# Kernel tuning notes

Hardware: AMD Instinct MI355X
Metric: run time of the kernel (lower is better)

## Reference

```python
import jax, jax.numpy as jnp
import numpy as np

D_MODEL = 1024
N_HEAD = 16
D_K = 64
D_V = 64
LN_EPS = 1e-5


def setup_inputs() -> dict:
    key = jax.random.key(0)
    ks = jax.random.split(key, 12)
    B, S = 4, 2048
    s = 1.0 / np.sqrt(D_MODEL)
    inp = {
        "q": jax.random.normal(ks[0], (B, S, D_MODEL), jnp.float32),
        "k": jax.random.normal(ks[1], (B, S, D_MODEL), jnp.float32),
        "v": jax.random.normal(ks[2], (B, S, D_MODEL), jnp.float32),
        "mask": jnp.ones((B, S, S), jnp.int32),
        "w_q": jax.random.normal(ks[3], (D_MODEL, N_HEAD * D_K), jnp.float32) * s,
        "b_q": jnp.zeros((N_HEAD * D_K,), jnp.float32),
        "w_k": jax.random.normal(ks[4], (D_MODEL, N_HEAD * D_K), jnp.float32) * s,
        "b_k": jnp.zeros((N_HEAD * D_K,), jnp.float32),
        "w_v": jax.random.normal(ks[5], (D_MODEL, N_HEAD * D_V), jnp.float32) * s,
        "b_v": jnp.zeros((N_HEAD * D_V,), jnp.float32),
        "w_fc": jax.random.normal(ks[6], (N_HEAD * D_V, D_MODEL), jnp.float32) * s,
        "b_fc": jnp.zeros((D_MODEL,), jnp.float32),
        "ln_g": jnp.ones((D_MODEL,), jnp.float32),
        "ln_b": jnp.zeros((D_MODEL,), jnp.float32),
    }
    return inp


def reference(q, k, v, mask, w_q, b_q, w_k, b_k, w_v, b_v, w_fc, b_fc, ln_g, ln_b):
    B, Sq, _ = q.shape
    Sk = k.shape[1]
    residual = q
    # QKV projections -> [B, H, S, d]
    qh = (q @ w_q + b_q).reshape(B, Sq, N_HEAD, D_K).transpose(0, 2, 1, 3)
    kh = (k @ w_k + b_k).reshape(B, Sk, N_HEAD, D_K).transpose(0, 2, 1, 3)
    vh = (v @ w_v + b_v).reshape(B, Sk, N_HEAD, D_V).transpose(0, 2, 1, 3)
    temp = jnp.sqrt(jnp.asarray(D_K, qh.dtype))
    scores = jnp.einsum("bhqd,bhkd->bhqk", qh / temp, kh)
    scores = jnp.where(mask[:, None, :, :] == 0, jnp.asarray(-1e9, scores.dtype), scores)
    attn = jax.nn.softmax(scores, axis=-1)  # dropout is identity in eval
    out = jnp.einsum("bhqk,bhkd->bhqd", attn, vh)
    out = out.transpose(0, 2, 1, 3).reshape(B, Sq, N_HEAD * D_V)
    out = out @ w_fc + b_fc  # output proj (dropout identity)
    x = out + residual
    mu = jnp.mean(x, axis=-1, keepdims=True)
    var = jnp.mean(jnp.square(x - mu), axis=-1, keepdims=True)
    y = (x - mu) * jax.lax.rsqrt(var + LN_EPS) * ln_g + ln_b
    return (y, attn)
```

## Files before the change

kernel.cpp:

```cpp
#include <hip/hip_runtime.h>
#include <cstdint>
#include <cstddef>

#define DM 1024
#define HN 16
#define DH 64
#define BB 4
#define SS 2048
#define MM (BB * SS)

typedef __bf16 bf16;
typedef bf16 bf16x8 __attribute__((ext_vector_type(8)));
typedef bf16 bf16x4 __attribute__((ext_vector_type(4)));
typedef float f32x4 __attribute__((ext_vector_type(4)));
typedef int i32x4 __attribute__((ext_vector_type(4)));

__device__ __forceinline__ f32x4 mfma16(bf16x8 a, bf16x8 b, f32x4 c) {
  return __builtin_amdgcn_mfma_f32_16x16x32_bf16(a, b, c, 0, 0, 0);
}

typedef __attribute__((address_space(3))) void lds_void_t;
typedef __attribute__((address_space(1))) void glob_void_t;

__device__ __forceinline__ void gload16(const void* g, void* l) {
  __builtin_amdgcn_global_load_lds((const glob_void_t*)g, (lds_void_t*)l, 16, 0, 0);
}

__global__ __launch_bounds__(256) void cvt3(const float* __restrict__ q,
                                            const float* __restrict__ k,
                                            const float* __restrict__ v,
                                            bf16* __restrict__ dst) {
  int which = blockIdx.y;
  const float* in = which == 0 ? q : which == 1 ? k : v;
  bf16* out = dst + (size_t)which * MM * DM;
  int i = (blockIdx.x * 256 + threadIdx.x) * 8;
  f32x4 a = *(const f32x4*)(in + i);
  f32x4 b = *(const f32x4*)(in + i + 4);
  bf16x8 o;
  o[0] = (bf16)a[0]; o[1] = (bf16)a[1]; o[2] = (bf16)a[2]; o[3] = (bf16)a[3];
  o[4] = (bf16)b[0]; o[5] = (bf16)b[1]; o[6] = (bf16)b[2]; o[7] = (bf16)b[3];
  *(bf16x8*)(out + i) = o;
}

__global__ __launch_bounds__(256) void wtrans4(const float* __restrict__ w_q,
                                               const float* __restrict__ w_k,
                                               const float* __restrict__ w_v,
                                               const float* __restrict__ w_fc,
                                               bf16* __restrict__ WT) {
  int p = blockIdx.z;
  const float* W = p == 0 ? w_q : p == 1 ? w_k : p == 2 ? w_v : w_fc;
  bf16* out = WT + (size_t)p * DM * DM;
  __shared__ float t[32][33];
  int n0 = blockIdx.x * 32, k0 = blockIdx.y * 32;
  int tid = threadIdx.x;
  int r = tid >> 3, c = (tid & 7) * 4;
  f32x4 v = *(const f32x4*)&W[(size_t)(k0 + r) * DM + n0 + c];
  t[r][c] = v[0]; t[r][c + 1] = v[1]; t[r][c + 2] = v[2]; t[r][c + 3] = v[3];
  __syncthreads();
  bf16x4 o;
#pragma unroll
  for (int i = 0; i < 4; ++i) o[i] = (bf16)t[c + i][r];
  *(bf16x4*)&out[(size_t)(n0 + r) * DM + k0 + c] = o;
}

__global__ __launch_bounds__(256) void gemm_qkv(const bf16* __restrict__ Abase,
                                                const bf16* __restrict__ Bt,
                                                const float* __restrict__ b_q,
                                                const float* __restrict__ b_k,
                                                const float* __restrict__ b_v,
                                                bf16* __restrict__ qhh,
                                                bf16* __restrict__ khh,
                                                bf16* __restrict__ vhT) {
  constexpr int K = DM;
  __shared__ bf16 Ab[128 * 32];
  __shared__ bf16 Bb[128 * 32];
  int tid = threadIdx.x, wave = tid >> 6, lane = tid & 63;
  int bm = blockIdx.x * 128, bn = blockIdx.y * 128;
  int proj = bn >> 10;
  const bf16* A = Abase + (size_t)proj * MM * DM;
  const float* bias = proj == 0 ? b_q : proj == 1 ? b_k : b_v;
  int wr = (wave >> 1) * 64, wc = (wave & 1) * 64;
  int fr = lane & 15, kg8 = (lane >> 4) * 8;
  f32x4 acc[4][4] = {};
  int arow = tid >> 2, acol = (tid & 3) * 8;
  const bf16* Ag0 = A + (size_t)(bm + arow) * K + acol;
  const bf16* Ag1 = Ag0 + (size_t)64 * K;
  const bf16* Bg0 = Bt + (size_t)(bn + arow) * K + acol;
  const bf16* Bg1 = Bg0 + (size_t)64 * K;
  char* la = (char*)Ab + wave * 1024;
  char* lb = (char*)Bb + wave * 1024;
  for (int k0 = 0; k0 < K; k0 += 32) {
    __syncthreads();
    gload16(Ag0 + k0, la);
    gload16(Ag1 + k0, la + 4096);
    gload16(Bg0 + k0, lb);
    gload16(Bg1 + k0, lb + 4096);
    asm volatile("s_waitcnt vmcnt(0)" ::: "memory");
    __syncthreads();
    bf16x8 af[4], bfr[4];
#pragma unroll
    for (int m = 0; m < 4; ++m)
      af[m] = *(const bf16x8*)&Ab[(wr + m * 16 + fr) * 32 + kg8];
#pragma unroll
    for (int n = 0; n < 4; ++n)
      bfr[n] = *(const bf16x8*)&Bb[(wc + n * 16 + fr) * 32 + kg8];
#pragma unroll
    for (int m = 0; m < 4; ++m)
#pragma unroll
      for (int n = 0; n < 4; ++n) acc[m][n] = mfma16(af[m], bfr[n], acc[m][n]);
  }
  int b = bm >> 11;
#pragma unroll
  for (int m = 0; m < 4; ++m)
#pragma unroll
    for (int n = 0; n < 4; ++n) {
      int c = bn + wc + n * 16 + fr;
      int lc = c & 1023;
      float bv = bias[lc];
      int h = lc >> 6, d = lc & 63;
      int r0 = bm + wr + m * 16 + (lane >> 4) * 4;
      int s0 = r0 & (SS - 1);
      if (proj == 2) {
        bf16x4 o;
#pragma unroll
        for (int j = 0; j < 4; ++j) o[j] = (bf16)(acc[m][n][j] + bv);
        *(bf16x4*)&vhT[((size_t)(b * HN + h) * DH + d) * SS + s0] = o;
      } else {
        bf16* dst = proj == 0 ? qhh : khh;
        float sc = proj == 0 ? 0.125f : 1.f;
#pragma unroll
        for (int j = 0; j < 4; ++j) {
          float v = (acc[m][n][j] + bv) * sc;
          dst[(size_t)(b * HN + h) * (SS * DH) + (size_t)(s0 + j) * DH + d] =
              (bf16)v;
        }
      }
    }
}

__global__ __launch_bounds__(256) void gemm_out(const bf16* __restrict__ A,
                                                const bf16* __restrict__ Bt,
                                                const float* __restrict__ bias,
                                                const float* __restrict__ resid,
                                                float* __restrict__ out) {
  constexpr int K = DM;
  __shared__ bf16 Ab[128 * 32];
  __shared__ bf16 Bb[128 * 32];
  int tid = threadIdx.x, wave = tid >> 6, lane = tid & 63;
  int bm = blockIdx.x * 128, bn = blockIdx.y * 128;
  int wr = (wave >> 1) * 64, wc = (wave & 1) * 64;
  int fr = lane & 15, kg8 = (lane >> 4) * 8;
  f32x4 acc[4][4] = {};
  int arow = tid >> 2, acol = (tid & 3) * 8;
  const bf16* Ag0 = A + (size_t)(bm + arow) * K + acol;
  const bf16* Ag1 = Ag0 + (size_t)64 * K;
  const bf16* Bg0 = Bt + (size_t)(bn + arow) * K + acol;
  const bf16* Bg1 = Bg0 + (size_t)64 * K;
  char* la = (char*)Ab + wave * 1024;
  char* lb = (char*)Bb + wave * 1024;
  for (int k0 = 0; k0 < K; k0 += 32) {
    __syncthreads();
    gload16(Ag0 + k0, la);
    gload16(Ag1 + k0, la + 4096);
    gload16(Bg0 + k0, lb);
    gload16(Bg1 + k0, lb + 4096);
    asm volatile("s_waitcnt vmcnt(0)" ::: "memory");
    __syncthreads();
    bf16x8 af[4], bfr[4];
#pragma unroll
    for (int m = 0; m < 4; ++m)
      af[m] = *(const bf16x8*)&Ab[(wr + m * 16 + fr) * 32 + kg8];
#pragma unroll
    for (int n = 0; n < 4; ++n)
      bfr[n] = *(const bf16x8*)&Bb[(wc + n * 16 + fr) * 32 + kg8];
#pragma unroll
    for (int m = 0; m < 4; ++m)
#pragma unroll
      for (int n = 0; n < 4; ++n) acc[m][n] = mfma16(af[m], bfr[n], acc[m][n]);
  }
#pragma unroll
  for (int m = 0; m < 4; ++m)
#pragma unroll
    for (int n = 0; n < 4; ++n) {
      int c = bn + wc + n * 16 + fr;
      float bv = bias[c];
#pragma unroll
      for (int j = 0; j < 4; ++j) {
        int r = bm + wr + m * 16 + (lane >> 4) * 4 + j;
        size_t idx = (size_t)r * DM + c;
        out[idx] = acc[m][n][j] + bv + resid[idx];
      }
    }
}

__global__ __launch_bounds__(512, 4) void attn_kernel(
    const bf16* __restrict__ qh, const bf16* __restrict__ kh,
    const bf16* __restrict__ vhT, const int* __restrict__ mask,
    float* __restrict__ attn_out, bf16* __restrict__ ctx) {
  extern __shared__ char smem[];
  float* pbuf = (float*)(smem + 16 * 4096);
  float* invp = (float*)(smem + 16 * 4096 + 4096);
  int tid = threadIdx.x, wave = tid >> 6, lane = tid & 63;
  int qt = blockIdx.x, bh = blockIdx.y;
  int b = bh >> 4, h = bh & 15;
  int q0 = qt * 16;
  const bf16* qbase = qh + ((size_t)bh * SS + q0) * DH;
  const bf16* kbase = kh + (size_t)bh * SS * DH;
  const bf16* vbase = vhT + (size_t)bh * SS * DH;
  int fr = lane & 15, kg = lane >> 4;

  bf16x8 qf0 = *(const bf16x8*)&qbase[(size_t)fr * DH + kg * 8];
  bf16x8 qf1 = *(const bf16x8*)&qbase[(size_t)fr * DH + 32 + kg * 8];

  {
    int sw = wave * 256;
    bf16x8 kb0[4], kb1[4];
    auto kload = [&](int g) {
      const bf16* kp = kbase + (size_t)(sw + g * 16 + fr) * DH + kg * 8;
      kb0[g & 3] = *(const bf16x8*)kp;
      kb1[g & 3] = *(const bf16x8*)(kp + 32);
    };
    kload(0);
    kload(1);
    kload(2);
#pragma unroll
    for (int g = 0; g < 16; ++g) {
      if (g < 13) kload(g + 3);
      f32x4 acc = {0.f, 0.f, 0.f, 0.f};
      acc = mfma16(qf0, kb0[g & 3], acc);
      acc = mfma16(qf1, kb1[g & 3], acc);
      int col = sw + g * 16 + fr;
      int slot = col >> 3, within = col & 7;
#pragma unroll
      for (int j = 0; j < 4; ++j) {
        int row = kg * 4 + j;
        *(bf16*)(smem + row * 4096 + ((slot ^ row) << 4) + within * 2) =
            (bf16)acc[j];
      }
    }
  }
  __syncthreads();

  {
    int row = wave * 2 + (lane >> 5);
    int la = lane & 31;
    char* rbase = smem + row * 4096;
    const int* mrow = mask + ((size_t)b * SS + q0 + row) * SS;
    float sum = 0.f;
#pragma unroll
    for (int it = 0; it < 8; ++it) {
      int slot = la + it * 32;
      char* p = rbase + ((slot ^ row) << 4);
      bf16x8 e = *(const bf16x8*)p;
      i32x4 ma = *(const i32x4*)&mrow[slot * 8];
      i32x4 mb = *(const i32x4*)&mrow[slot * 8 + 4];
      bf16x8 w8;
#pragma unroll
      for (int i = 0; i < 4; ++i) {
        float f = __expf((float)e[i]);
        f = (ma[i] == 0) ? 0.f : f;
        sum += f;
        w8[i] = (bf16)f;
      }
#pragma unroll
      for (int i = 0; i < 4; ++i) {
        float f = __expf((float)e[i + 4]);
        f = (mb[i] == 0) ? 0.f : f;
        sum += f;
        w8[i + 4] = (bf16)f;
      }
      *(bf16x8*)p = w8;
    }
#pragma unroll
    for (int off = 1; off < 32; off <<= 1) sum += __shfl_xor(sum, off);
    float inv = 1.f / sum;
    if (la == 0) invp[row] = inv;
    float* arow_ = attn_out + ((size_t)bh * SS + q0 + row) * SS;
#pragma unroll
    for (int it = 0; it < 8; ++it) {
      int slot = la + it * 32;
      bf16x8 e = *(const bf16x8*)(rbase + ((slot ^ row) << 4));
      f32x4 u0, u1;
#pragma unroll
      for (int i = 0; i < 4; ++i) {
        u0[i] = (float)e[i] * inv;
        u1[i] = (float)e[i + 4] * inv;
      }
      __builtin_nontemporal_store(u0, (f32x4*)&arow_[slot * 8]);
      __builtin_nontemporal_store(u1, (f32x4*)&arow_[slot * 8 + 4]);
    }
  }
  __syncthreads();

  {
    int dq = wave & 3, khalf = wave >> 2;
    f32x4 cacc = {0.f, 0.f, 0.f, 0.f};
    const bf16* vrow = vbase + (size_t)(dq * 16 + fr) * SS + khalf * 1024;
    char* prow = smem + fr * 4096;
    bf16x8 vb[4], pb[4];
    auto pvload = [&](int kk) {
      vb[kk & 3] = *(const bf16x8*)&vrow[kk * 32 + kg * 8];
      int slotA = khalf * 128 + kk * 4 + kg;
      pb[kk & 3] = *(const bf16x8*)(prow + ((slotA ^ fr) << 4));
    };
    pvload(0);
    pvload(1);
    pvload(2);
#pragma unroll
    for (int kk = 0; kk < 32; ++kk) {
      if (kk < 29) pvload(kk + 3);
      cacc = mfma16(pb[kk & 3], vb[kk & 3], cacc);
    }
    if (khalf == 1) {
#pragma unroll
      for (int j = 0; j < 4; ++j)
        pbuf[dq * 256 + (kg * 4 + j) * 16 + fr] = cacc[j];
    }
    __syncthreads();
    if (khalf == 0) {
#pragma unroll
      for (int j = 0; j < 4; ++j) {
        int row = kg * 4 + j;
        float v = (cacc[j] + pbuf[dq * 256 + row * 16 + fr]) * invp[row];
        ctx[((size_t)b * SS + q0 + row) * DM + h * DH + dq * 16 + fr] = (bf16)v;
      }
    }
  }
}

__global__ __launch_bounds__(256) void ln_k(float* __restrict__ x,
                                            const float* __restrict__ g,
                                            const float* __restrict__ bln) {
  int r = blockIdx.x, tid = threadIdx.x;
  f32x4 v = *(const f32x4*)&x[(size_t)r * DM + tid * 4];
  float s = v[0] + v[1] + v[2] + v[3];
  float s2 = v[0] * v[0] + v[1] * v[1] + v[2] * v[2] + v[3] * v[3];
#pragma unroll
  for (int off = 32; off; off >>= 1) {
    s += __shfl_down(s, off);
    s2 += __shfl_down(s2, off);
  }
  __shared__ float rs_[4], rs2_[4];
  int wave = tid >> 6, lane = tid & 63;
  if (lane == 0) {
    rs_[wave] = s;
    rs2_[wave] = s2;
  }
  __syncthreads();
  s = rs_[0] + rs_[1] + rs_[2] + rs_[3];
  s2 = rs2_[0] + rs2_[1] + rs2_[2] + rs2_[3];
  float mu = s * (1.f / DM);
  float var = s2 * (1.f / DM) - mu * mu;
  float rstd = rsqrtf(var + 1e-5f);
  f32x4 gg = *(const f32x4*)&g[tid * 4];
  f32x4 bb = *(const f32x4*)&bln[tid * 4];
  f32x4 o;
#pragma unroll
  for (int i = 0; i < 4; ++i) o[i] = (v[i] - mu) * rstd * gg[i] + bb[i];
  *(f32x4*)&x[(size_t)r * DM + tid * 4] = o;
}

extern "C" void kernel_launch(void* const* d_in, const int* in_sizes, int n_in,
                              void* d_out, int out_size, void* d_ws,
                              size_t ws_size, hipStream_t stream) {
  const float* q = (const float*)d_in[0];
  const float* k = (const float*)d_in[1];
  const float* v = (const float*)d_in[2];
  const int* mask = (const int*)d_in[3];
  const float* w_q = (const float*)d_in[4];
  const float* b_q = (const float*)d_in[5];
  const float* w_k = (const float*)d_in[6];
  const float* b_k = (const float*)d_in[7];
  const float* w_v = (const float*)d_in[8];
  const float* b_v = (const float*)d_in[9];
  const float* w_fc = (const float*)d_in[10];
  const float* b_fc = (const float*)d_in[11];
  const float* ln_g = (const float*)d_in[12];
  const float* ln_b = (const float*)d_in[13];

  float* y = (float*)d_out;
  float* attn_out = (float*)d_out + (size_t)MM * DM;

  char* w = (char*)d_ws;
  const size_t actN = (size_t)MM * DM;
  bf16* qkv_bf = (bf16*)w;  w += 3 * actN * 2;
  bf16* wT = (bf16*)w;      w += (size_t)4 * DM * DM * 2;
  bf16* qhh = (bf16*)w;     w += actN * 2;
  bf16* khh = (bf16*)w;     w += actN * 2;
  bf16* vhT = (bf16*)w;     w += actN * 2;
  bf16* ctx = (bf16*)w;     w += actN * 2;

  cvt3<<<dim3(4096, 3), 256, 0, stream>>>(q, k, v, qkv_bf);
  wtrans4<<<dim3(DM / 32, DM / 32, 4), 256, 0, stream>>>(w_q, w_k, w_v, w_fc, wT);
  gemm_qkv<<<dim3(MM / 128, 3072 / 128), 256, 0, stream>>>(
      qkv_bf, wT, b_q, b_k, b_v, qhh, khh, vhT);
  hipFuncSetAttribute((const void*)attn_kernel,
                      hipFuncAttributeMaxDynamicSharedMemorySize, 69696);
  attn_kernel<<<dim3(SS / 16, BB * HN), 512, 69696, stream>>>(
      qhh, khh, vhT, mask, attn_out, ctx);
  gemm_out<<<dim3(MM / 128, DM / 128), 256, 0, stream>>>(
      ctx, wT + (size_t)3 * DM * DM, b_fc, q, y);
  ln_k<<<MM, 256, 0, stream>>>(y, ln_g, ln_b);
}
```

Before: 759.0 us.

## Restructure attention: bit-packed mask, 32-row tiles, in-register softmax, staged PV pipeline

A new pre-pass packs the int32 mask into per-column 32-bit words, one bit per query row, so the attention kernel reads 4 bytes per column instead of 128 bytes of mask. The attention kernel now handles 32 query rows per block and keeps the exponentiated scores in registers instead of writing raw scores to LDS and re-reading them. It then stages P through two LDS buffers in chunks and interleaves the fp32 attn writes with the PV MFMAs. V is stored in 32-column tiles and blocks are remapped so the 8 blocks of each residue group work on the same batch-head. In exchange this adds an extra kernel launch, higher register pressure, and plain stores where nontemporal stores were used before.

Result: slower. 1.599 ms (+110.6%).

```diff
diff --git a/kernel.cpp b/kernel.cpp
--- a/kernel.cpp
+++ b/kernel.cpp
@@ -24,6 +24,26 @@
 
 __device__ __forceinline__ void gload16(const void* g, void* l) {
   __builtin_amdgcn_global_load_lds((const glob_void_t*)g, (lds_void_t*)l, 16, 0, 0);
+}
+
+__global__ __launch_bounds__(256) void mask_bitsT(const int* __restrict__ mask,
+                                                  unsigned int* __restrict__ mT) {
+  int qt = blockIdx.x, b = blockIdx.y;
+  int col0 = threadIdx.x * 8;
+  unsigned int m[8] = {0, 0, 0, 0, 0, 0, 0, 0};
+  const int* mp = mask + ((size_t)b * SS + qt * 32) * SS + col0;
+  for (int r = 0; r < 32; ++r) {
+    i32x4 a = *(const i32x4*)(mp + (size_t)r * SS);
+    i32x4 c = *(const i32x4*)(mp + (size_t)r * SS + 4);
+#pragma unroll
+    for (int i = 0; i < 4; ++i) {
+      m[i] |= (unsigned int)(a[i] != 0) << r;
+      m[4 + i] |= (unsigned int)(c[i] != 0) << r;
+    }
+  }
+#pragma unroll
+  for (int i = 0; i < 8; ++i)
+    mT[((size_t)b * 64 + qt) * SS + col0 + i] = m[i];
 }
 
 __global__ __launch_bounds__(256) void cvt3(const float* __restrict__ q,
@@ -124,7 +144,8 @@
         bf16x4 o;
 #pragma unroll
         for (int j = 0; j < 4; ++j) o[j] = (bf16)(acc[m][n][j] + bv);
-        *(bf16x4*)&vhT[((size_t)(b * HN + h) * DH + d) * SS + s0] = o;
+        *(bf16x4*)&vhT[(size_t)(b * HN + h) * (SS * DH) +
+                       (size_t)(s0 >> 5) * (DH * 32) + d * 32 + (s0 & 31)] = o;
       } else {
         bf16* dst = proj == 0 ? qhh : khh;
         float sc = proj == 0 ? 0.125f : 1.f;
@@ -195,25 +216,33 @@
 
 __global__ __launch_bounds__(512, 4) void attn_kernel(
     const bf16* __restrict__ qh, const bf16* __restrict__ kh,
-    const bf16* __restrict__ vhT, const int* __restrict__ mask,
+    const bf16* __restrict__ vhT, const unsigned int* __restrict__ mT,
     float* __restrict__ attn_out, bf16* __restrict__ ctx) {
   extern __shared__ char smem[];
-  float* pbuf = (float*)(smem + 16 * 4096);
-  float* invp = (float*)(smem + 16 * 4096 + 4096);
+  char* staged0 = smem;
+  char* staged1 = smem + 32768;
+  float* wsum = (float*)(smem + 65536);
+  float* invp = (float*)(smem + 65536 + 1024);
   int tid = threadIdx.x, wave = tid >> 6, lane = tid & 63;
-  int qt = blockIdx.x, bh = blockIdx.y;
+  int fid = (blockIdx.x & 7) * 512 + (blockIdx.x >> 3);
+  int bh = fid >> 6, qt = fid & 63;
   int b = bh >> 4, h = bh & 15;
-  int q0 = qt * 16;
+  int q0 = qt * 32;
   const bf16* qbase = qh + ((size_t)bh * SS + q0) * DH;
   const bf16* kbase = kh + (size_t)bh * SS * DH;
   const bf16* vbase = vhT + (size_t)bh * SS * DH;
+  const unsigned int* mTb = mT + ((size_t)b * 64 + qt) * SS;
   int fr = lane & 15, kg = lane >> 4;
 
-  bf16x8 qf0 = *(const bf16x8*)&qbase[(size_t)fr * DH + kg * 8];
-  bf16x8 qf1 = *(const bf16x8*)&qbase[(size_t)fr * DH + 32 + kg * 8];
-
+  bf16x8 qa0 = *(const bf16x8*)&qbase[(size_t)fr * DH + kg * 8];
+  bf16x8 qa1 = *(const bf16x8*)&qbase[(size_t)fr * DH + 32 + kg * 8];
+  bf16x8 qb0 = *(const bf16x8*)&qbase[(size_t)(16 + fr) * DH + kg * 8];
+  bf16x8 qb1 = *(const bf16x8*)&qbase[(size_t)(16 + fr) * DH + 32 + kg * 8];
+
+  bf16x4 pa[16], pb[16];
+  float rs[8] = {0.f, 0.f, 0.f, 0.f, 0.f, 0.f, 0.f, 0.f};
+  int sw = wave * 256;
   {
-    int sw = wave * 256;
     bf16x8 kb0[4], kb1[4];
     auto kload = [&](int g) {
       const bf16* kp = kbase + (size_t)(sw + g * 16 + fr) * DH + kg * 8;
@@ -226,105 +255,109 @@
 #pragma unroll
     for (int g = 0; g < 16; ++g) {
       if (g < 13) kload(g + 3);
-      f32x4 acc = {0.f, 0.f, 0.f, 0.f};
-      acc = mfma16(qf0, kb0[g & 3], acc);
-      acc = mfma16(qf1, kb1[g & 3], acc);
-      int col = sw + g * 16 + fr;
-      int slot = col >> 3, within = col & 7;
+      f32x4 aa = {0.f, 0.f, 0.f, 0.f};
+      f32x4 ab = {0.f, 0.f, 0.f, 0.f};
+      aa = mfma16(qa0, kb0[g & 3], aa);
+      aa = mfma16(qa1, kb1[g & 3], aa);
+      ab = mfma16(qb0, kb0[g & 3], ab);
+      ab = mfma16(qb1, kb1[g & 3], ab);
+      unsigned int bits = mTb[sw + g * 16 + fr];
 #pragma unroll
       for (int j = 0; j < 4; ++j) {
-        int row = kg * 4 + j;
-        *(bf16*)(smem + row * 4096 + ((slot ^ row) << 4) + within * 2) =
-            (bf16)acc[j];
-      }
+        float fa = ((bits >> (kg * 4 + j)) & 1u) ? __expf(aa[j]) : 0.f;
+        float fb = ((bits >> (16 + kg * 4 + j)) & 1u) ? __expf(ab[j]) : 0.f;
+        rs[j] += fa;
+        rs[4 + j] += fb;
+        pa[g][j] = (bf16)fa;
+        pb[g][j] = (bf16)fb;
+      }
+    }
+  }
+#pragma unroll
+  for (int j = 0; j < 8; ++j) {
+#pragma unroll
+    for (int off = 1; off < 16; off <<= 1) rs[j] += __shfl_xor(rs[j], off);
+  }
+  if (fr == 0) {
+#pragma unroll
+    for (int j = 0; j < 4; ++j) {
+      wsum[wave * 32 + kg * 4 + j] = rs[j];
+      wsum[wave * 32 + 16 + kg * 4 + j] = rs[4 + j];
     }
   }
   __syncthreads();
-
+  if (tid < 32) {
+    float s = 0.f;
+#pragma unroll
+    for (int w = 0; w < 8; ++w) s += wsum[w * 32 + tid];
+    invp[tid] = 1.f / s;
+  }
+  __syncthreads();
+
+  auto stage = [&](char* buf) {
+    int base = (wave & 1) * 256;
+#pragma unroll
+    for (int g = 0; g < 16; ++g) {
+      int lcol = base + g * 16 + fr;
+      int slot = lcol >> 3, w2 = (lcol & 7) * 2;
+#pragma unroll
+      for (int j = 0; j < 4; ++j) {
+        int rowA = kg * 4 + j, rowB = rowA + 16;
+        *(bf16*)(buf + rowA * 1024 + ((slot ^ (rowA & 7)) << 4) + w2) = pa[g][j];
+        *(bf16*)(buf + rowB * 1024 + ((slot ^ (rowB & 7)) << 4) + w2) = pb[g][j];
+      }
+    }
+  };
+
+  f32x4 cacc = {0.f, 0.f, 0.f, 0.f};
+  int rb = wave >> 2, dq = wave & 3;
+  int prow_row = rb * 16 + fr;
+  int pr7 = prow_row & 7;
   {
-    int row = wave * 2 + (lane >> 5);
-    int la = lane & 31;
-    char* rbase = smem + row * 4096;
-    const int* mrow = mask + ((size_t)b * SS + q0 + row) * SS;
-    float sum = 0.f;
-#pragma unroll
-    for (int it = 0; it < 8; ++it) {
-      int slot = la + it * 32;
-      char* p = rbase + ((slot ^ row) << 4);
-      bf16x8 e = *(const bf16x8*)p;
-      i32x4 ma = *(const i32x4*)&mrow[slot * 8];
-      i32x4 mb = *(const i32x4*)&mrow[slot * 8 + 4];
-      bf16x8 w8;
-#pragma unroll
-      for (int i = 0; i < 4; ++i) {
-        float f = __expf((float)e[i]);
-        f = (ma[i] == 0) ? 0.f : f;
-        sum += f;
-        w8[i] = (bf16)f;
-      }
-#pragma unroll
-      for (int i = 0; i < 4; ++i) {
-        float f = __expf((float)e[i + 4]);
-        f = (mb[i] == 0) ? 0.f : f;
-        sum += f;
-        w8[i + 4] = (bf16)f;
-      }
-      *(bf16x8*)p = w8;
-    }
-#pragma unroll
-    for (int off = 1; off < 32; off <<= 1) sum += __shfl_xor(sum, off);
-    float inv = 1.f / sum;
-    if (la == 0) invp[row] = inv;
-    float* arow_ = attn_out + ((size_t)bh * SS + q0 + row) * SS;
-#pragma unroll
-    for (int it = 0; it < 8; ++it) {
-      int slot = la + it * 32;
-      bf16x8 e = *(const bf16x8*)(rbase + ((slot ^ row) << 4));
-      f32x4 u0, u1;
-#pragma unroll
-      for (int i = 0; i < 4; ++i) {
-        u0[i] = (float)e[i] * inv;
-        u1[i] = (float)e[i + 4] * inv;
-      }
-      __builtin_nontemporal_store(u0, (f32x4*)&arow_[slot * 8]);
-      __builtin_nontemporal_store(u1, (f32x4*)&arow_[slot * 8 + 4]);
-    }
-  }
-  __syncthreads();
-
-  {
-    int dq = wave & 3, khalf = wave >> 2;
-    f32x4 cacc = {0.f, 0.f, 0.f, 0.f};
-    const bf16* vrow = vbase + (size_t)(dq * 16 + fr) * SS + khalf * 1024;
-    char* prow = smem + fr * 4096;
-    bf16x8 vb[4], pb[4];
-    auto pvload = [&](int kk) {
-      vb[kk & 3] = *(const bf16x8*)&vrow[kk * 32 + kg * 8];
-      int slotA = khalf * 128 + kk * 4 + kg;
-      pb[kk & 3] = *(const bf16x8*)(prow + ((slotA ^ fr) << 4));
-    };
-    pvload(0);
-    pvload(1);
-    pvload(2);
-#pragma unroll
-    for (int kk = 0; kk < 32; ++kk) {
-      if (kk < 29) pvload(kk + 3);
-      cacc = mfma16(pb[kk & 3], vb[kk & 3], cacc);
-    }
-    if (khalf == 1) {
-#pragma unroll
-      for (int j = 0; j < 4; ++j)
-        pbuf[dq * 256 + (kg * 4 + j) * 16 + fr] = cacc[j];
-    }
-    __syncthreads();
-    if (khalf == 0) {
-#pragma unroll
-      for (int j = 0; j < 4; ++j) {
-        int row = kg * 4 + j;
-        float v = (cacc[j] + pbuf[dq * 256 + row * 16 + fr]) * invp[row];
-        ctx[((size_t)b * SS + q0 + row) * DM + h * DH + dq * 16 + fr] = (bf16)v;
-      }
-    }
+    if ((wave >> 1) == 0) stage(staged0);
+    __syncthreads();
+  }
+#pragma unroll
+  for (int c = 0; c < 4; ++c) {
+    char* buf = (c & 1) ? staged1 : staged0;
+    char* nbuf = (c & 1) ? staged0 : staged1;
+    if (c < 3 && (wave >> 1) == c + 1) stage(nbuf);
+    {
+      int row = tid >> 4, colg = tid & 15;
+      float inv = invp[row];
+      float* orow = attn_out + ((size_t)bh * SS + q0 + row) * SS + c * 512;
+      char* srow = buf + row * 1024;
+      int r7 = row & 7;
+#pragma unroll
+      for (int i = 0; i < 8; ++i) {
+        int col = i * 64 + colg * 4;
+        bf16x4 e =
+            *(const bf16x4*)(srow + (((col >> 3) ^ r7) << 4) + (col & 7) * 2);
+        f32x4 u = {(float)e[0] * inv, (float)e[1] * inv, (float)e[2] * inv,
+                   (float)e[3] * inv};
+        *(f32x4*)(orow + col) = u;
+      }
+    }
+    {
+      const bf16* vt = vbase + (size_t)(c * 16) * (DH * 32) +
+                       (dq * 16 + fr) * 32 + kg * 8;
+      char* prow = buf + prow_row * 1024;
+#pragma unroll
+      for (int kk = 0; kk < 16; ++kk) {
+        bf16x8 pafr =
+            *(const bf16x8*)(prow + (((kk * 4 + kg) ^ pr7) << 4));
+        bf16x8 vf = *(const bf16x8*)&vt[(size_t)kk * (DH * 32)];
+        cacc = mfma16(pafr, vf, cacc);
+      }
+    }
+    __syncthreads();
+  }
+
+#pragma unroll
+  for (int j = 0; j < 4; ++j) {
+    int row = rb * 16 + kg * 4 + j;
+    float v = cacc[j] * invp[row];
+    ctx[((size_t)b * SS + q0 + row) * DM + h * DH + dq * 16 + fr] = (bf16)v;
   }
 }
 
@@ -389,15 +422,17 @@
   bf16* khh = (bf16*)w;     w += actN * 2;
   bf16* vhT = (bf16*)w;     w += actN * 2;
   bf16* ctx = (bf16*)w;     w += actN * 2;
-
+  unsigned int* mT = (unsigned int*)w;  w += (size_t)BB * 64 * SS * 4;
+
+  mask_bitsT<<<dim3(SS / 32, BB), 256, 0, stream>>>(mask, mT);
   cvt3<<<dim3(4096, 3), 256, 0, stream>>>(q, k, v, qkv_bf);
   wtrans4<<<dim3(DM / 32, DM / 32, 4), 256, 0, stream>>>(w_q, w_k, w_v, w_fc, wT);
   gemm_qkv<<<dim3(MM / 128, 3072 / 128), 256, 0, stream>>>(
       qkv_bf, wT, b_q, b_k, b_v, qhh, khh, vhT);
   hipFuncSetAttribute((const void*)attn_kernel,
-                      hipFuncAttributeMaxDynamicSharedMemorySize, 69696);
-  attn_kernel<<<dim3(SS / 16, BB * HN), 512, 69696, stream>>>(
-      qhh, khh, vhT, mask, attn_out, ctx);
+                      hipFuncAttributeMaxDynamicSharedMemorySize, 66688);
+  attn_kernel<<<4096, 512, 66688, stream>>>(
+      qhh, khh, vhT, mT, attn_out, ctx);
   gemm_out<<<dim3(MM / 128, DM / 128), 256, 0, stream>>>(
       ctx, wT + (size_t)3 * DM * DM, b_fc, q, y);
   ln_k<<<MM, 256, 0, stream>>>(y, ln_g, ln_b);
```
